# Optimization experiments

Measured on AMD Instinct MI355X. Metric: run time of the kernel, lower is better.

## Reference

```python
import jax, jax.numpy as jnp
import numpy as np

D_MODEL = 1024


def setup_inputs() -> dict:
    key = jax.random.key(0)
    ks = jax.random.split(key, 7)
    s = 1.0 / np.sqrt(D_MODEL)
    return {
        "x": jax.random.normal(ks[0], (4, 4096, D_MODEL), dtype=jnp.float32),
        "Wq": jax.random.normal(ks[1], (D_MODEL, D_MODEL), dtype=jnp.float32) * s,
        "bq": jax.random.normal(ks[2], (D_MODEL,), dtype=jnp.float32) * s,
        "Wk": jax.random.normal(ks[3], (D_MODEL, D_MODEL), dtype=jnp.float32) * s,
        "bk": jax.random.normal(ks[4], (D_MODEL,), dtype=jnp.float32) * s,
        "Wv": jax.random.normal(ks[5], (D_MODEL, D_MODEL), dtype=jnp.float32) * s,
        "bv": jax.random.normal(ks[6], (D_MODEL,), dtype=jnp.float32) * s,
    }


def reference(x, Wq, bq, Wk, bk, Wv, bv):
    # nn.Linear: y = x @ W.T + b
    Q = jnp.einsum("bsd,ed->bse", x, Wq) + bq  # [B,S,D]
    K = jnp.einsum("bsd,ed->bse", x, Wk) + bk
    V = jnp.einsum("bsd,ed->bse", x, Wv) + bv
    scale = 1.0 / jnp.sqrt(jnp.asarray(x.shape[-1], dtype=x.dtype))
    KV = jnp.einsum("bsd,bse->bde", K, V) * scale  # [B,D,D]
    E = jnp.einsum("bsd,bde->bse", Q, KV)  # [B,S,D]
    return E
```

## Files before the change

### kernel.cpp

```cpp
#include <hip/hip_runtime.h>
#include <hip/hip_fp16.h>


#define BATCH 4
#define SEQ   4096
#define DM    1024

typedef _Float16 h8 __attribute__((ext_vector_type(8)));
typedef _Float16 h4 __attribute__((ext_vector_type(4)));
typedef float    f4 __attribute__((ext_vector_type(4)));

__device__ inline void gload_lds16(const _Float16* g, _Float16* l) {
    __builtin_amdgcn_global_load_lds(
        (const __attribute__((address_space(1))) void*)g,
        (__attribute__((address_space(3))) void*)l,
        16, 0, 0);
}

__device__ inline int xcd_swz(int bid, int grid) {
    const int q = grid >> 3;
    return (bid & 7) * q + (bid >> 3);
}

__device__ inline float doth(const _Float16* wr, const float* v, int lane) {
    float s = 0.f;
    #pragma unroll
    for (int i = 0; i < 2; ++i) {
        const int k = i * 512 + lane * 8;
        h8 wv = *(const h8*)&wr[k];
        f4 v0 = *(const f4*)&v[k];
        f4 v1 = *(const f4*)&v[k + 4];
        s += (float)wv[0] * v0.x + (float)wv[1] * v0.y +
             (float)wv[2] * v0.z + (float)wv[3] * v0.w +
             (float)wv[4] * v1.x + (float)wv[5] * v1.y +
             (float)wv[6] * v1.z + (float)wv[7] * v1.w;
    }
    return s;
}
__device__ inline float dotf(const float* a, const float* b, int lane) {
    float s = 0.f;
    #pragma unroll
    for (int i = 0; i < 4; ++i) {
        const int k = i * 256 + lane * 4;
        f4 x = *(const f4*)&a[k];
        f4 y = *(const f4*)&b[k];
        s += x.x * y.x + x.y * y.y + x.z * y.z + x.w * y.w;
    }
    return s;
}
__device__ inline float wred(float s) {
    #pragma unroll
    for (int off = 32; off; off >>= 1) s += __shfl_down(s, off);
    return s;
}

__global__ __launch_bounds__(256) void cvt_all(
    const float* __restrict__ x, const float* __restrict__ Wq,
    const float* __restrict__ Wk, const float* __restrict__ Wv,
    _Float16* __restrict__ xt, _Float16* __restrict__ xh,
    _Float16* __restrict__ Wqt, _Float16* __restrict__ Wkt,
    _Float16* __restrict__ Wvh, float* __restrict__ xs)
{
    __shared__ float tile[64][65];
    __shared__ float red[4][64];
    const int bid = blockIdx.x;
    const int t   = threadIdx.x;
    const int tr  = t >> 4;
    const int tc  = (t & 15) * 4;

    const float* src;
    _Float16 *dstT = nullptr, *dstRM = nullptr;
    int r0, c0, C, R;
    bool isX = bid < 4096;
    if (isX) {
        const int b  = bid >> 10;
        const int tt = bid & 1023;
        r0 = (tt >> 4) * 64; c0 = (tt & 15) * 64;
        R = SEQ; C = DM;
        src   = x  + (long)b * SEQ * DM;
        dstT  = xt + (long)b * SEQ * DM;
        dstRM = xh + (long)b * SEQ * DM;
        xs   += b * DM;
    } else {
        const int wb = bid - 4096;
        const int z  = wb >> 8;
        const int tt = wb & 255;
        r0 = (tt >> 4) * 64; c0 = (tt & 15) * 64;
        R = DM; C = DM;
        src = z == 0 ? Wq : (z == 1 ? Wk : Wv);
        if (z == 0) dstT = Wqt;
        else if (z == 1) dstT = Wkt;
        else dstRM = Wvh;
    }

    #pragma unroll
    for (int i = 0; i < 4; ++i) {
        const int r = tr + i * 16;
        f4 v = *(const f4*)&src[(long)(r0 + r) * C + c0 + tc];
        tile[r][tc + 0] = v.x; tile[r][tc + 1] = v.y;
        tile[r][tc + 2] = v.z; tile[r][tc + 3] = v.w;
        if (dstRM) {
            h4 h = { (_Float16)v.x, (_Float16)v.y, (_Float16)v.z, (_Float16)v.w };
            *(h4*)&dstRM[(long)(r0 + r) * C + c0 + tc] = h;
        }
    }
    __syncthreads();
    if (dstT) {
        #pragma unroll
        for (int i = 0; i < 4; ++i) {
            const int c = tr + i * 16;
            h4 h = { (_Float16)tile[tc + 0][c], (_Float16)tile[tc + 1][c],
                     (_Float16)tile[tc + 2][c], (_Float16)tile[tc + 3][c] };
            *(h4*)&dstT[(long)(c0 + c) * R + r0 + tc] = h;
        }
    }
    if (isX) {
        const int cc = t & 63;
        const int rb = (t >> 6) * 16;
        float ps = 0.f;
        #pragma unroll
        for (int r = 0; r < 16; ++r) ps += tile[rb + r][cc];
        red[t >> 6][cc] = ps;
        __syncthreads();
        if (t < 64)
            atomicAdd(&xs[c0 + t], red[0][t] + red[1][t] + red[2][t] + red[3][t]);
    }
}

__global__ __launch_bounds__(256) void gemv_misc(
    const _Float16* __restrict__ Wvh, const _Float16* __restrict__ Wqt,
    const _Float16* __restrict__ Wkt,
    const float* __restrict__ xs, const float* __restrict__ bv,
    const float* __restrict__ bk, const float* __restrict__ bq,
    float* __restrict__ u2, float* __restrict__ qk,
    float* __restrict__ kb)
{
    const int gw   = blockIdx.x * 4 + (threadIdx.x >> 6);
    const int lane = threadIdx.x & 63;
    if (gw < 4096) {
        float s = wred(doth(Wvh + (long)(gw & 1023) * DM, xs + (gw >> 10) * DM, lane));
        if (lane == 0) u2[gw] = s + (float)SEQ * bv[gw & 1023];
    } else if (gw < 5120) {
        float s = wred(doth(Wqt + (long)(gw - 4096) * DM, bk, lane));
        if (lane == 0) qk[gw - 4096] = s;
    } else {
        float s = wred(doth(Wkt + (long)(gw - 5120) * DM, bq, lane));
        if (lane == 0) kb[gw - 5120] = s;
    }
}

__global__ __launch_bounds__(256) void gemv_cvqw(
    const _Float16* __restrict__ Ph, const _Float16* __restrict__ Mh,
    const float* __restrict__ kb, const float* __restrict__ xs,
    const float* __restrict__ u2, const float* __restrict__ bv,
    const float* __restrict__ sv,
    float* __restrict__ cv, float* __restrict__ qw)
{
    const int gw   = blockIdx.x * 4 + (threadIdx.x >> 6);
    const int lane = threadIdx.x & 63;
    if (gw < 4096) {
        const int b = gw >> 10;
        const int e = gw & 1023;
        float s = wred(doth(Ph + (long)b * DM * DM + (long)e * DM, kb, lane));
        if (lane == 0)
            cv[gw] = s + (sv[0] * u2[gw] + sv[1 + b] * bv[e]) * 0.03125f;
    } else {
        const int g = gw - 4096;
        const int b = g >> 10;
        const int i = g & 1023;
        float s = wred(doth(Mh + (long)i * DM, xs + b * DM, lane));
        if (lane == 0) qw[g] = s;
    }
}

__global__ __launch_bounds__(256) void reduce_tri(
    const _Float16* __restrict__ parts, _Float16* __restrict__ Gh,
    const float* __restrict__ kb, const float* __restrict__ xs,
    const float* __restrict__ bq, const float* __restrict__ bk,
    float* __restrict__ sv)
{
    const int bid = blockIdx.x;
    if (bid == 640) {
        const int wv   = threadIdx.x >> 6;
        const int lane = threadIdx.x & 63;
        float s = wred(dotf(kb, xs + wv * DM, lane));
        if (lane == 0) sv[1 + wv] = s;
        if (wv == 0) {
            float s0 = wred(dotf(bq, bk, lane));
            if (lane == 0) sv[0] = s0;
        }
        return;
    }
    __shared__ _Float16 lds[64][72];
    const int job = bid >> 4;
    const int ch  = bid & 15;
    const int b   = job / 10;
    const int p   = job - b * 10;
    const int ti  = p >= 6 ? 3 : (p >= 3 ? 2 : (p >= 1 ? 1 : 0));
    const int tj  = p - ((ti * (ti + 1)) >> 1);
    const int li  = (ch >> 2) * 64;
    const int lj  = (ch & 3) * 64;
    const int t   = threadIdx.x;
    const int c8  = (t & 7) * 8;
    const long DD_ = (long)DM * DM;

    h8 o[2];
    #pragma unroll
    for (int h = 0; h < 2; ++h) {
        const int r = (t >> 3) + h * 32;
        float a[8] = {};
        #pragma unroll
        for (int s = 0; s < 6; ++s) {
            const _Float16* src = parts + ((long)(job * 6 + s) << 16);
            h8 v = *(const h8*)&src[(li + r) * 256 + lj + c8];
            #pragma unroll
            for (int j = 0; j < 8; ++j) a[j] += (float)v[j];
        }
        #pragma unroll
        for (int j = 0; j < 8; ++j) o[h][j] = (_Float16)(a[j] * 0.03125f);
        *(h8*)&Gh[b * DD_ + (long)(ti * 256 + li + r) * DM + tj * 256 + lj + c8] = o[h];
        *(h8*)&lds[r][c8] = o[h];
    }
    if (ti != tj) {
        __syncthreads();
        #pragma unroll
        for (int h = 0; h < 2; ++h) {
            const int r = (t >> 3) + h * 32;
            h8 m;
            #pragma unroll
            for (int j = 0; j < 8; ++j) m[j] = lds[c8 + j][r];
            *(h8*)&Gh[b * DD_ + (long)(tj * 256 + lj + r) * DM + ti * 256 + li + c8] = m;
        }
    }
}

template<typename OutT, int BIAS, int TRI>
__global__ __launch_bounds__(512, 1) void gemm8p(
    const _Float16* __restrict__ A, const _Float16* __restrict__ B,
    OutT* __restrict__ C,
    int K, int lda, int ldb, int ldc, int tilesX, int perZ,
    long aZ, long bZ, long cZ, int sk, long aK, long bK,
    const float* __restrict__ bc1, long bc1Z, float alpha)
{
    __shared__ _Float16 lds[2 * 32768];

    const int L = xcd_swz(blockIdx.x, gridDim.x);
    int tileM, tileN, cTileM, cTileN, NT;
    const float* pc1 = nullptr;
    if (TRI) {
        const int job = L / 6;
        const int s   = L - job * 6;
        const int b   = job / 10;
        const int p   = job - b * 10;
        const int ti  = p >= 6 ? 3 : (p >= 3 ? 2 : (p >= 1 ? 1 : 0));
        const int tj  = p - ((ti * (ti + 1)) >> 1);
        const int kOff = s < 4 ? s * 704 : 2816 + (s - 4) * 640;
        NT = s < 4 ? 11 : 10;
        A += (long)b * aZ + kOff;
        B += (long)b * aZ + kOff;
        C += (long)(job * 6 + s) * cZ;
        tileM = ti * 256; tileN = tj * 256;
        cTileM = 0; cTileN = 0;
    } else {
        const int z  = L / perZ;
        const int r0 = L - z * perZ;
        const int zb = z / sk;
        const int zk = z - zb * sk;
        A += (long)zb * aZ + (long)zk * aK;
        B += (long)zb * bZ + (long)zk * bK;
        C += (long)z * cZ;
        if (BIAS == 1) pc1 = bc1 + (long)zb * bc1Z;
        tileM = (r0 / tilesX) * 256;
        tileN = (r0 % tilesX) * 256;
        cTileM = tileM; cTileN = tileN;
        NT = K >> 6;
    }

    const int tid  = threadIdx.x;
    const int lane = tid & 63;
    const int wave = tid >> 6;
    const int wr   = wave >> 2;
    const int wc   = wave & 3;
    const int la   = lane & 15;
    const int kg   = lane >> 4;

    auto stageA = [&](int buf, int mq, int kt) {
        _Float16* dst = &lds[buf * 32768 + mq * 8192];
        const int k0 = kt * 64;
        #pragma unroll
        for (int i = 0; i < 2; ++i) {
            const int U = i * 512 + tid;
            const int R = U >> 3, s = U & 7;
            const int gr = tileM + (R >> 6) * 128 + mq * 64 + (R & 63);
            gload_lds16(&A[(long)gr * lda + k0 + ((s ^ (R & 7)) << 3)], dst + U * 8);
        }
    };
    auto stageB = [&](int buf, int nq, int kt) {
        _Float16* dst = &lds[buf * 32768 + 16384 + nq * 8192];
        const int k0 = kt * 64;
        #pragma unroll
        for (int i = 0; i < 2; ++i) {
            const int U = i * 512 + tid;
            const int R = U >> 3, s = U & 7;
            const int gn = tileN + (R >> 5) * 64 + nq * 32 + (R & 31);
            gload_lds16(&B[(long)gn * ldb + k0 + ((s ^ (R & 7)) << 3)], dst + U * 8);
        }
    };

    f4 acc[8][4] = {};
    h8 af[4][2];
    h8 bf[2][2][2];

    auto readA = [&](int buf, int mq) {
        const _Float16* Ab = &lds[buf * 32768 + mq * 8192];
        #pragma unroll
        for (int mi = 0; mi < 4; ++mi)
            #pragma unroll
            for (int kk = 0; kk < 2; ++kk) {
                const int R = wr * 64 + mi * 16 + la;
                const int s = kk * 4 + kg;
                af[mi][kk] = *(const h8*)&Ab[R * 64 + ((s ^ (R & 7)) << 3)];
            }
    };
    auto readB = [&](int buf, int nq) {
        const _Float16* Bb = &lds[buf * 32768 + 16384 + nq * 8192];
        #pragma unroll
        for (int ni = 0; ni < 2; ++ni)
            #pragma unroll
            for (int kk = 0; kk < 2; ++kk) {
                const int R = wc * 32 + ni * 16 + la;
                const int s = kk * 4 + kg;
                bf[nq][ni][kk] = *(const h8*)&Bb[R * 64 + ((s ^ (R & 7)) << 3)];
            }
    };
    auto mfmaQ = [&](int mq, int nq) {
        __builtin_amdgcn_s_setprio(1);
        #pragma unroll
        for (int mi = 0; mi < 4; ++mi)
            #pragma unroll
            for (int ni = 0; ni < 2; ++ni)
                #pragma unroll
                for (int kk = 0; kk < 2; ++kk)
                    acc[mq * 4 + mi][nq * 2 + ni] =
                        __builtin_amdgcn_mfma_f32_16x16x32_f16(
                            af[mi][kk], bf[nq][ni][kk],
                            acc[mq * 4 + mi][nq * 2 + ni], 0, 0, 0);
        __builtin_amdgcn_s_setprio(0);
    };

    stageA(0, 0, 0); stageA(0, 1, 0); stageB(0, 0, 0); stageB(0, 1, 0);
    if (NT > 1) {
        stageA(1, 0, 1); stageB(1, 0, 1);
        asm volatile("s_waitcnt vmcnt(4)" ::: "memory");
    } else {
        asm volatile("s_waitcnt vmcnt(0)" ::: "memory");
    }
    __builtin_amdgcn_sched_barrier(0);
    __builtin_amdgcn_s_barrier();

    for (int j = 0; j < NT; ++j) {
        const int buf = j & 1;
        readA(buf, 0); readB(buf, 0);
        if (j + 1 < NT) stageA(buf ^ 1, 1, j + 1);
        asm volatile("s_waitcnt lgkmcnt(8)" ::: "memory");
        __builtin_amdgcn_s_barrier();
        asm volatile("s_waitcnt lgkmcnt(0)" ::: "memory");
        __builtin_amdgcn_sched_barrier(0);
        mfmaQ(0, 0);
        __builtin_amdgcn_s_barrier();
        readB(buf, 1);
        if (j + 1 < NT) stageB(buf ^ 1, 1, j + 1);
        __builtin_amdgcn_s_barrier();
        asm volatile("s_waitcnt lgkmcnt(0)" ::: "memory");
        __builtin_amdgcn_sched_barrier(0);
        mfmaQ(0, 1);
        __builtin_amdgcn_s_barrier();
        readA(buf, 1);
        if (j + 2 < NT) stageA(buf, 0, j + 2);
        __builtin_amdgcn_s_barrier();
        asm volatile("s_waitcnt lgkmcnt(0)" ::: "memory");
        __builtin_amdgcn_sched_barrier(0);
        mfmaQ(1, 0);
        __builtin_amdgcn_s_barrier();
        if (j + 2 < NT) stageB(buf, 0, j + 2);
        __builtin_amdgcn_s_barrier();
        mfmaQ(1, 1);
        if (j + 2 < NT) {
            asm volatile("s_waitcnt vmcnt(4)" ::: "memory");
        } else if (j + 1 < NT) {
            asm volatile("s_waitcnt vmcnt(0)" ::: "memory");
        }
        __builtin_amdgcn_sched_barrier(0);
        __builtin_amdgcn_s_barrier();
    }

    #pragma unroll
    for (int mf = 0; mf < 8; ++mf) {
        #pragma unroll
        for (int nf = 0; nf < 4; ++nf) {
            const int col = cTileN + wc * 64 + nf * 16 + la;
            #pragma unroll
            for (int jj = 0; jj < 4; ++jj) {
                const int row = cTileM + wr * 128 + mf * 16 + kg * 4 + jj;
                float v = acc[mf][nf][jj] * alpha;
                if (BIAS == 1) v += pc1[col];
                C[(long)row * ldc + col] = (OutT)v;
            }
        }
    }
}

template<int BIAS>
__global__ __launch_bounds__(256) void gemm64(
    const _Float16* __restrict__ A, const _Float16* __restrict__ B,
    _Float16* __restrict__ C,
    const _Float16* __restrict__ A2, const _Float16* __restrict__ B2,
    _Float16* __restrict__ C2, int zSplit,
    int K, int lda, int ldb, int ldc, int tilesX, int perZ,
    long aZ, long bZ, long cZ,
    const float* __restrict__ bc1, long bc1Z,
    const float* __restrict__ br1, long br1Z,
    const float* __restrict__ bc2, long bc2Z,
    const float* __restrict__ br2, long br2Z,
    float alpha, float beta)
{
    __shared__ _Float16 As[64 * 64];
    __shared__ _Float16 Bs[64 * 64];

    const int L  = xcd_swz(blockIdx.x, gridDim.x);
    int z        = L / perZ;
    const int r0 = L - z * perZ;
    if (z >= zSplit) { A = A2; B = B2; C = C2; z = 0; }
    A += (long)z * aZ;
    B += (long)z * bZ;
    C += (long)z * cZ;
    const float* pc1 = nullptr; const float* pr1 = nullptr;
    const float* pc2 = nullptr; const float* pr2 = nullptr;
    if (BIAS == 3) {
        pc1 = bc1 + (long)z * bc1Z; pr1 = br1 + (long)z * br1Z;
        pc2 = bc2 + (long)z * bc2Z; pr2 = br2 + (long)z * br2Z;
    }

    const int tileM = (r0 / tilesX) * 64;
    const int tileN = (r0 % tilesX) * 64;
    const int tid   = threadIdx.x;
    const int lane  = tid & 63;
    const int wave  = tid >> 6;
    const int wm    = (wave >> 1) * 32;
    const int wn    = (wave & 1) * 32;
    const int srow  = tid >> 3;
    const int sslot = tid & 7;

    f4 acc[2][2] = {};
    const int arow = lane & 15;
    const int kg   = lane >> 4;

    for (int k0 = 0; k0 < K; k0 += 64) {
        #pragma unroll
        for (int i = 0; i < 2; ++i) {
            const int row   = i * 32 + srow;
            const int gslot = sslot ^ (row & 7);
            gload_lds16(&A[(long)(tileM + row) * lda + k0 + gslot * 8],
                        &As[row * 64 + sslot * 8]);
            gload_lds16(&B[(long)(tileN + row) * ldb + k0 + gslot * 8],
                        &Bs[row * 64 + sslot * 8]);
        }
        __syncthreads();

        #pragma unroll
        for (int kk = 0; kk < 64; kk += 32) {
            h8 af[2], bf[2];
            #pragma unroll
            for (int m = 0; m < 2; ++m) {
                const int rr   = wm + m * 16 + arow;
                const int slot = (kk >> 3) + kg;
                af[m] = *(const h8*)&As[rr * 64 + ((slot ^ (rr & 7)) << 3)];
            }
            #pragma unroll
            for (int n = 0; n < 2; ++n) {
                const int rr   = wn + n * 16 + arow;
                const int slot = (kk >> 3) + kg;
                bf[n] = *(const h8*)&Bs[rr * 64 + ((slot ^ (rr & 7)) << 3)];
            }
            #pragma unroll
            for (int m = 0; m < 2; ++m)
                #pragma unroll
                for (int n = 0; n < 2; ++n)
                    acc[m][n] = __builtin_amdgcn_mfma_f32_16x16x32_f16(
                        af[m], bf[n], acc[m][n], 0, 0, 0);
        }
        __syncthreads();
    }

    #pragma unroll
    for (int m = 0; m < 2; ++m) {
        #pragma unroll
        for (int n = 0; n < 2; ++n) {
            const int col = tileN + wn + n * 16 + arow;
            #pragma unroll
            for (int j = 0; j < 4; ++j) {
                const int row = tileM + wm + m * 16 + (lane >> 4) * 4 + j;
                float v = acc[m][n][j] * alpha;
                if (BIAS == 3) v += beta * (pc1[col] * pr1[row] + pc2[col] * pr2[row]);
                C[(long)row * ldc + col] = (_Float16)v;
            }
        }
    }
}

extern "C" void kernel_launch(void* const* d_in, const int* in_sizes, int n_in,
                              void* d_out, int out_size, void* d_ws, size_t ws_size,
                              hipStream_t stream)
{
    const float* x  = (const float*)d_in[0];
    const float* Wq = (const float*)d_in[1];
    const float* bq = (const float*)d_in[2];
    const float* Wk = (const float*)d_in[3];
    const float* bk = (const float*)d_in[4];
    const float* Wv = (const float*)d_in[5];
    const float* bv = (const float*)d_in[6];
    float* out = (float*)d_out;

    const long DD = (long)DM * DM;
    const long DS = (long)DM * SEQ;
    const long MB = 1024l * 1024;

    char* base = (char*)d_ws;
    _Float16* xh   = (_Float16*)base;
    _Float16* xt   = (_Float16*)(base + 32 * MB);
    _Float16* Gh   = xt;
    _Float16* Ph   = (_Float16*)(base + 40 * MB);
    _Float16* Rth  = (_Float16*)(base + 48 * MB);
    _Float16* Wqt  = (_Float16*)(base + 64 * MB);
    _Float16* Wvh  = (_Float16*)(base + 66 * MB);
    _Float16* Wkt  = (_Float16*)(base + 68 * MB);
    _Float16* Mh   = (_Float16*)(base + 70 * MB);
    float*    vecs = (float*)(base + 72 * MB);
    float*    u2   = vecs;
    float*    qk   = vecs + 4096;
    float*    kb   = vecs + 5120;
    float*    xs   = vecs + 6144;
    float*    qw   = vecs + 10240;
    float*    cv   = vecs + 14336;
    float*    sv   = vecs + 18432;
    _Float16* parts = (_Float16*)d_out;

    hipMemsetAsync(xs, 0, BATCH * DM * sizeof(float), stream);

    cvt_all<<<4864, 256, 0, stream>>>(x, Wq, Wk, Wv, xt, xh, Wqt, Wkt, Wvh, xs);

    gemv_misc<<<1536, 256, 0, stream>>>(Wvh, Wqt, Wkt, xs, bv, bk, bq, u2, qk, kb);

    gemm8p<_Float16, 0, 1><<<240, 512, 0, stream>>>(
        xt, xt, parts, 4096, SEQ, SEQ, 256, 0, 0,
        DS, DS, 65536, 1, 0, 0, nullptr, 0, 1.0f);

    reduce_tri<<<641, 256, 0, stream>>>(parts, Gh, kb, xs, bq, bk, sv);

    gemm64<0><<<1280, 256, 0, stream>>>(
        Wvh, Gh, Ph, Wqt, Wkt, Mh, 4,
        1024, DM, DM, DM, 16, 256,
        0, DD, DD,
        nullptr, 0, nullptr, 0, nullptr, 0, nullptr, 0, 1.0f, 0.f);

    gemv_cvqw<<<2048, 256, 0, stream>>>(Ph, Mh, kb, xs, u2, bv, sv, cv, qw);

    gemm64<3><<<1024, 256, 0, stream>>>(
        Ph, Mh, Rth, nullptr, nullptr, nullptr, 99,
        1024, DM, DM, DM, 16, 256,
        DD, 0, DD,
        qk, 0, u2, 1024, qw, 1024, bv, 0, 1.0f, 0.03125f);

    gemm8p<float, 1, 0><<<256, 512, 0, stream>>>(
        xh, Rth, out, 1024, DM, DM, DM, 4, 64,
        DS, DD, DS, 1, 0, 0, cv, 1024, 1.0f);
}
```

Measured before the change: 149.7 us.

## Batch GEMV weight rows across four vectors and prefetch B fragments earlier in gemm8p

New measurement: 152.0 us. About the same (+1.5%).

```diff
diff --git a/kernel.cpp b/kernel.cpp
--- a/kernel.cpp
+++ b/kernel.cpp
@@ -36,6 +36,23 @@
              (float)wv[6] * v1.z + (float)wv[7] * v1.w;
     }
     return s;
+}
+__device__ inline void doth4(const _Float16* wr, const float* xs, int lane, float* s) {
+    #pragma unroll
+    for (int i = 0; i < 2; ++i) {
+        const int k = i * 512 + lane * 8;
+        h8 wv = *(const h8*)&wr[k];
+        #pragma unroll
+        for (int b = 0; b < 4; ++b) {
+            const float* v = xs + b * DM + k;
+            f4 v0 = *(const f4*)&v[0];
+            f4 v1 = *(const f4*)&v[4];
+            s[b] += (float)wv[0] * v0.x + (float)wv[1] * v0.y +
+                    (float)wv[2] * v0.z + (float)wv[3] * v0.w +
+                    (float)wv[4] * v1.x + (float)wv[5] * v1.y +
+                    (float)wv[6] * v1.z + (float)wv[7] * v1.w;
+        }
+    }
 }
 __device__ inline float dotf(const float* a, const float* b, int lane) {
     float s = 0.f;
@@ -137,15 +154,20 @@
 {
     const int gw   = blockIdx.x * 4 + (threadIdx.x >> 6);
     const int lane = threadIdx.x & 63;
-    if (gw < 4096) {
-        float s = wred(doth(Wvh + (long)(gw & 1023) * DM, xs + (gw >> 10) * DM, lane));
-        if (lane == 0) u2[gw] = s + (float)SEQ * bv[gw & 1023];
-    } else if (gw < 5120) {
-        float s = wred(doth(Wqt + (long)(gw - 4096) * DM, bk, lane));
-        if (lane == 0) qk[gw - 4096] = s;
-    } else {
-        float s = wred(doth(Wkt + (long)(gw - 5120) * DM, bq, lane));
-        if (lane == 0) kb[gw - 5120] = s;
+    if (gw < 1024) {
+        float s[4] = {};
+        doth4(Wvh + (long)gw * DM, xs, lane, s);
+        #pragma unroll
+        for (int b = 0; b < 4; ++b) {
+            float r = wred(s[b]);
+            if (lane == 0) u2[b * DM + gw] = r + (float)SEQ * bv[gw];
+        }
+    } else if (gw < 2048) {
+        float s = wred(doth(Wqt + (long)(gw - 1024) * DM, bk, lane));
+        if (lane == 0) qk[gw - 1024] = s;
+    } else if (gw < 3072) {
+        float s = wred(doth(Wkt + (long)(gw - 2048) * DM, bq, lane));
+        if (lane == 0) kb[gw - 2048] = s;
     }
 }
 
@@ -164,12 +186,15 @@
         float s = wred(doth(Ph + (long)b * DM * DM + (long)e * DM, kb, lane));
         if (lane == 0)
             cv[gw] = s + (sv[0] * u2[gw] + sv[1 + b] * bv[e]) * 0.03125f;
-    } else {
-        const int g = gw - 4096;
-        const int b = g >> 10;
-        const int i = g & 1023;
-        float s = wred(doth(Mh + (long)i * DM, xs + b * DM, lane));
-        if (lane == 0) qw[g] = s;
+    } else if (gw < 5120) {
+        const int i = gw - 4096;
+        float s[4] = {};
+        doth4(Mh + (long)i * DM, xs, lane, s);
+        #pragma unroll
+        for (int b = 0; b < 4; ++b) {
+            float r = wred(s[b]);
+            if (lane == 0) qw[b * DM + i] = r;
+        }
     }
 }
 
@@ -357,12 +382,12 @@
     }
     __builtin_amdgcn_sched_barrier(0);
     __builtin_amdgcn_s_barrier();
+    readB(0, 0);
 
     for (int j = 0; j < NT; ++j) {
         const int buf = j & 1;
-        readA(buf, 0); readB(buf, 0);
+        readA(buf, 0);
         if (j + 1 < NT) stageA(buf ^ 1, 1, j + 1);
-        asm volatile("s_waitcnt lgkmcnt(8)" ::: "memory");
         __builtin_amdgcn_s_barrier();
         asm volatile("s_waitcnt lgkmcnt(0)" ::: "memory");
         __builtin_amdgcn_sched_barrier(0);
@@ -381,7 +406,14 @@
         asm volatile("s_waitcnt lgkmcnt(0)" ::: "memory");
         __builtin_amdgcn_sched_barrier(0);
         mfmaQ(1, 0);
-        __builtin_amdgcn_s_barrier();
+        if (j + 2 < NT) {
+            asm volatile("s_waitcnt vmcnt(6)" ::: "memory");
+        } else if (j + 1 < NT) {
+            asm volatile("s_waitcnt vmcnt(4)" ::: "memory");
+        }
+        __builtin_amdgcn_sched_barrier(0);
+        __builtin_amdgcn_s_barrier();
+        if (j + 1 < NT) readB(buf ^ 1, 0);
         if (j + 2 < NT) stageB(buf, 0, j + 2);
         __builtin_amdgcn_s_barrier();
         mfmaQ(1, 1);
@@ -549,7 +581,7 @@
 
     cvt_all<<<4864, 256, 0, stream>>>(x, Wq, Wk, Wv, xt, xh, Wqt, Wkt, Wvh, xs);
 
-    gemv_misc<<<1536, 256, 0, stream>>>(Wvh, Wqt, Wkt, xs, bv, bk, bq, u2, qk, kb);
+    gemv_misc<<<768, 256, 0, stream>>>(Wvh, Wqt, Wkt, xs, bv, bk, bq, u2, qk, kb);
 
     gemm8p<_Float16, 0, 1><<<240, 512, 0, stream>>>(
         xt, xt, parts, 4096, SEQ, SEQ, 256, 0, 0,
@@ -563,7 +595,7 @@
         0, DD, DD,
         nullptr, 0, nullptr, 0, nullptr, 0, nullptr, 0, 1.0f, 0.f);
 
-    gemv_cvqw<<<2048, 256, 0, stream>>>(Ph, Mh, kb, xs, u2, bv, sv, cv, qw);
+    gemv_cvqw<<<1280, 256, 0, stream>>>(Ph, Mh, kb, xs, u2, bv, sv, cv, qw);
 
     gemm64<3><<<1024, 256, 0, stream>>>(
         Ph, Mh, Rth, nullptr, nullptr, nullptr, 99,
```
